# Kernel optimization log

Hardware: AMD Instinct MI355X
Metric: run time of the kernel (lower is better)

## Reference

```python
import jax, jax.numpy as jnp
import numpy as np

D_STATE = 16
D_CONV = 4


def mamba(u, in_w, conv_w, conv_b, x_w, dt_w, dt_b, A_log, Dp, out_w):
    """Standard Mamba block. u: (B, L, d_model)."""
    Bsz, L, _ = u.shape
    xz = u @ in_w.T                      # (B, L, 2*d_inner)
    d_in = xz.shape[-1] // 2
    x, z = xz[..., :d_in], xz[..., d_in:]
    # causal depthwise conv along L
    xt = x.transpose(0, 2, 1)            # (B, d_in, L)
    k = conv_w[:, None, :]               # (d_in, 1, d_conv)
    xt = jax.lax.conv_general_dilated(xt, k, (1,), [(D_CONV - 1, 0)],
                                      feature_group_count=d_in)
    x = jax.nn.silu(xt.transpose(0, 2, 1) + conv_b)
    dbl = x @ x_w.T                      # (B, L, dt_rank + 2*d_state)
    dt_rank = dt_w.shape[1]
    dt = jax.nn.softplus(dbl[..., :dt_rank] @ dt_w.T + dt_b)  # (B, L, d_in)
    Bm = dbl[..., dt_rank:dt_rank + D_STATE]                   # (B, L, n)
    Cm = dbl[..., dt_rank + D_STATE:]                          # (B, L, n)
    A = -jnp.exp(A_log)                                        # (d_in, n)
    dA = jnp.exp(jnp.einsum('bld,dn->bldn', dt, A))            # (B, L, d_in, n)
    dBu = jnp.einsum('bld,bln->bldn', dt * x, Bm)              # (B, L, d_in, n)

    def step(h, inp):
        dA_t, dBu_t, C_t = inp
        h = dA_t * h + dBu_t                                   # (B, d_in, n)
        y = jnp.einsum('bdn,bn->bd', h, C_t)
        return h, y

    h0 = jnp.zeros((Bsz, d_in, D_STATE), u.dtype)
    _, ys = jax.lax.scan(step, h0, (dA.transpose(1, 0, 2, 3),
                                    dBu.transpose(1, 0, 2, 3),
                                    Cm.transpose(1, 0, 2)))
    y = ys.transpose(1, 0, 2) + x * Dp                         # skip connection
    y = y * jax.nn.silu(z)
    return y @ out_w.T


def _mamba_params(key, d_model):
    d_in = 2 * d_model
    dt_rank = max(1, -(-d_model // 16))
    ks = jax.random.split(key, 6)
    s = lambda n: 1.0 / np.sqrt(n)
    p = {
        'in_w': jax.random.normal(ks[0], (2 * d_in, d_model)) * s(d_model),
        'conv_w': jax.random.normal(ks[1], (d_in, D_CONV)) * s(D_CONV),
        'conv_b': jnp.zeros((d_in,)),
        'x_w': jax.random.normal(ks[2], (dt_rank + 2 * D_STATE, d_in)) * s(d_in),
        'dt_w': jax.random.normal(ks[3], (d_in, dt_rank)) * s(dt_rank),
        'dt_b': jax.random.uniform(ks[4], (d_in,), minval=-4.0, maxval=-2.0),
        'A_log': jnp.log(jnp.tile(jnp.arange(1.0, D_STATE + 1.0)[None, :], (d_in, 1))),
        'D': jnp.ones((d_in,)),
        'out_w': jax.random.normal(ks[5], (d_model, d_in)) * s(d_in),
    }
    return p


def setup_inputs() -> dict:
    key = jax.random.key(0)
    kf1, kf2, km1, km2 = jax.random.split(key, 4)
    B, C, H, W = 4, 32, 64, 64
    inp = {
        'fo1': jax.random.normal(kf1, (B, C, H, W), jnp.float32),
        'fo2': jax.random.normal(kf2, (B, C, H, W), jnp.float32),
    }
    for pref, kk, dm in (('m1_', km1, 4 * C), ('m2_', km2, 2)):
        for name, v in _mamba_params(kk, dm).items():
            inp[pref + name] = v.astype(jnp.float32)
    return inp


def reference(fo1, fo2,
              m1_in_w, m1_conv_w, m1_conv_b, m1_x_w, m1_dt_w, m1_dt_b, m1_A_log, m1_D, m1_out_w,
              m2_in_w, m2_conv_w, m2_conv_b, m2_x_w, m2_dt_w, m2_dt_b, m2_A_log, m2_D, m2_out_w):
    B, C, H, W = fo1.shape
    # four directional line-scan sequences, each (B, H*W, C)
    h_fwd = fo1.reshape(B, C, H * W).transpose(0, 2, 1)
    h_bwd = jnp.flip(h_fwd, axis=1)
    w_fwd = fo1.transpose(0, 1, 3, 2).reshape(B, C, H * W).transpose(0, 2, 1)
    w_bwd = jnp.flip(w_fwd, axis=1)
    fop = jnp.concatenate([h_fwd, h_bwd, w_fwd, w_bwd], axis=2)   # (B, HW, 4C)
    fop = mamba(fop, m1_in_w, m1_conv_w, m1_conv_b, m1_x_w, m1_dt_w,
                m1_dt_b, m1_A_log, m1_D, m1_out_w)
    fop = fop.reshape(B, H * W, 4, C).sum(2)                      # (B, HW, C)
    fop = fop.transpose(0, 2, 1).reshape(B, C, H, W)
    residual = fop * fo2
    foc = residual.mean(axis=(2, 3)).reshape(B, C, 1)             # adaptive avg pool (1,1)
    foc = jnp.concatenate([foc, jnp.flip(foc, axis=1)], axis=2)   # (B, C, 2)
    foc = mamba(foc, m2_in_w, m2_conv_w, m2_conv_b, m2_x_w, m2_dt_w,
                m2_dt_b, m2_A_log, m2_D, m2_out_w)
    foc = foc.sum(2, keepdims=True)[..., None]                    # (B, C, 1, 1)
    return foc * residual + residual
```

## Files before the change

kernel.cpp:

```cpp
#include <hip/hip_runtime.h>
#include <cstdint>
#include <cstddef>

constexpr int NCH = 128;
constexpr int TCH = 32;

typedef __attribute__((ext_vector_type(8))) short bf16x8;
typedef __attribute__((ext_vector_type(4))) float f32x4;

static __device__ __forceinline__ float sigm_(float x) { return 1.0f / (1.0f + __expf(-x)); }
static __device__ __forceinline__ float silu_(float x) { return x * sigm_(x); }
static __device__ __forceinline__ float softplus_(float x) { return (x > 20.0f) ? x : log1pf(__expf(x)); }
static __device__ __forceinline__ unsigned short f2bf(float f) {
    union { float f; unsigned int u; } v; v.f = f;
    unsigned int r = v.u + 0x7FFFu + ((v.u >> 16) & 1u);
    return (unsigned short)(r >> 16);
}

__global__ void k_prep(const float* __restrict__ alog1, const float* __restrict__ alog2,
                       const float* __restrict__ w_in, const float* __restrict__ w_x,
                       const float* __restrict__ w_o,
                       float* __restrict__ A2m1, float* __restrict__ A2m2,
                       unsigned short* __restrict__ win_bf, unsigned short* __restrict__ wx_bf,
                       unsigned short* __restrict__ wo_bf, float* __restrict__ foc0) {
    int i = blockIdx.x * 256 + threadIdx.x;
    const float LOG2E = 1.4426950408889634f;
    if (i < 4096)        A2m1[i] = -__expf(alog1[i]) * LOG2E;
    else if (i < 4160)   A2m2[i - 4096] = -__expf(alog2[i - 4096]) * LOG2E;
    else if (i < 69696)  win_bf[i - 4160]  = f2bf(w_in[i - 4160]);
    else if (i < 79936)  wx_bf[i - 69696]  = f2bf(w_x[i - 69696]);
    else if (i < 112704) wo_bf[i - 79936]  = f2bf(w_o[i - 79936]);
    else if (i < 112832) foc0[i - 112704]  = 0.0f;
}

__global__ __launch_bounds__(256) void k_gather(const float* __restrict__ fo1, unsigned short* __restrict__ u) {
    __shared__ float lds[32][65];
    int blk = blockIdx.x;
    int b = blk >> 6, h = blk & 63;
    int tid = threadIdx.x;
    {
        int w = tid & 63, cs = tid >> 6;
        const float* src = fo1 + (size_t)(b * 32) * 4096 + h * 64 + w;
        #pragma unroll
        for (int j = 0; j < 8; ++j) {
            int c = cs * 8 + j;
            lds[c][w] = src[(size_t)c * 4096];
        }
    }
    __syncthreads();
    {
        int c = tid & 31, wsub = tid >> 5;
        #pragma unroll
        for (int j = 0; j < 8; ++j) {
            int w = wsub * 8 + j;
            unsigned short v = f2bf(lds[c][w]);
            int l  = h * 64 + w;
            int l2 = w * 64 + h;
            u[(size_t)(b * 4096 + l)        * 128 +       c] = v;
            u[(size_t)(b * 4096 + 4095 - l) * 128 + 32  + c] = v;
            u[(size_t)(b * 4096 + l2)       * 128 + 64  + c] = v;
            u[(size_t)(b * 4096 + 4095 - l2)* 128 + 96  + c] = v;
        }
    }
}

__global__ __launch_bounds__(256) void k_gemm_mfma(const unsigned short* __restrict__ A,
                                                   const unsigned short* __restrict__ W,
                                                   float* __restrict__ Cmat, int M, int N, int K) {
    __shared__ unsigned short As[128][40];
    __shared__ unsigned short Ws[128][40];
    int n0 = blockIdx.x * 128, m0 = blockIdx.y * 128;
    int tid = threadIdx.x;
    int lane = tid & 63, wv = tid >> 6;
    int mh = wv >> 1, nh = wv & 1;
    int lm = lane & 15, quad = lane >> 4;

    f32x4 acc[4][4];
    #pragma unroll
    for (int i = 0; i < 4; ++i)
        #pragma unroll
        for (int j = 0; j < 4; ++j) acc[i][j] = (f32x4)(0.0f);

    for (int k0 = 0; k0 < K; k0 += 32) {
        #pragma unroll
        for (int j = 0; j < 2; ++j) {
            int c = tid + 256 * j;
            int row = c >> 2;
            int kc = (c & 3) * 8;
            uint4 av = *(const uint4*)&A[(size_t)(m0 + row) * K + k0 + kc];
            *(uint4*)&As[row][kc] = av;
            uint4 wvv = make_uint4(0u, 0u, 0u, 0u);
            if (n0 + row < N) wvv = *(const uint4*)&W[(size_t)(n0 + row) * K + k0 + kc];
            *(uint4*)&Ws[row][kc] = wvv;
        }
        __syncthreads();
        bf16x8 a_frag[4], b_frag[4];
        #pragma unroll
        for (int i = 0; i < 4; ++i)
            a_frag[i] = *(const bf16x8*)&As[mh * 64 + 16 * i + lm][quad * 8];
        #pragma unroll
        for (int j = 0; j < 4; ++j)
            b_frag[j] = *(const bf16x8*)&Ws[nh * 64 + 16 * j + lm][quad * 8];
        #pragma unroll
        for (int i = 0; i < 4; ++i)
            #pragma unroll
            for (int j = 0; j < 4; ++j)
                acc[i][j] = __builtin_amdgcn_mfma_f32_16x16x32_bf16(a_frag[i], b_frag[j], acc[i][j], 0, 0, 0);
        __syncthreads();
    }
    #pragma unroll
    for (int i = 0; i < 4; ++i) {
        #pragma unroll
        for (int r = 0; r < 4; ++r) {
            size_t mrow = (size_t)(m0 + mh * 64 + 16 * i + quad * 4 + r) * N;
            #pragma unroll
            for (int j = 0; j < 4; ++j) {
                int col = n0 + nh * 64 + 16 * j + lm;
                if (col < N) Cmat[mrow + col] = acc[i][j][r];
            }
        }
    }
}

__global__ __launch_bounds__(256) void k_conv(const float* __restrict__ xz, const float* __restrict__ cw,
                                              const float* __restrict__ cb, float* __restrict__ x,
                                              unsigned short* __restrict__ xbf) {
    int blk = blockIdx.x;
    int b = blk >> 7, lc = blk & 127;
    int d = threadIdx.x;
    int l0 = lc * 32;
    float w0 = cw[d * 4 + 0], w1 = cw[d * 4 + 1], w2 = cw[d * 4 + 2], w3 = cw[d * 4 + 3];
    float bb = cb[d];
    size_t rbase = ((size_t)(b * 4096 + l0)) * 512 + d;
    float xm1 = (l0 >= 1) ? xz[rbase - 512]  : 0.f;
    float xm2 = (l0 >= 2) ? xz[rbase - 1024] : 0.f;
    float xm3 = (l0 >= 3) ? xz[rbase - 1536] : 0.f;
    size_t wbase = ((size_t)(b * 4096 + l0)) * 256 + d;
    for (int il = 0; il < 32; ++il) {
        float xc = xz[rbase + (size_t)il * 512];
        float v = silu_(bb + w3 * xc + w2 * xm1 + w1 * xm2 + w0 * xm3);
        x[wbase + (size_t)il * 256] = v;
        xbf[wbase + (size_t)il * 256] = f2bf(v);
        xm3 = xm2; xm2 = xm1; xm1 = xc;
    }
}

__global__ __launch_bounds__(256) void k_scan1(const float* __restrict__ x, const float* __restrict__ dbl,
                                               const float* __restrict__ A2, const float* __restrict__ dtw,
                                               const float* __restrict__ dtb,
                                               float* __restrict__ P, float* __restrict__ S) {
    int blk = blockIdx.x;
    int b = blk / NCH, ch = blk % NCH;
    int d = threadIdx.x;
    float wdt[8];
    #pragma unroll
    for (int r = 0; r < 8; ++r) wdt[r] = dtw[d * 8 + r];
    float bdt = dtb[d];
    float a2[16], h[16], p[16];
    #pragma unroll
    for (int n = 0; n < 16; ++n) { a2[n] = A2[d * 16 + n]; h[n] = 0.f; p[n] = 1.f; }
    int t0 = ch * TCH;
    for (int t = t0; t < t0 + TCH; ++t) {
        size_t row = (size_t)(b * 4096 + t);
        const float* br = dbl + row * 40;
        float4 q0 = *(const float4*)(br), q1 = *(const float4*)(br + 4);
        float4 b0 = *(const float4*)(br + 8), b1 = *(const float4*)(br + 12),
               b2 = *(const float4*)(br + 16), b3 = *(const float4*)(br + 20);
        float dtv = softplus_(q0.x * wdt[0] + q0.y * wdt[1] + q0.z * wdt[2] + q0.w * wdt[3] +
                              q1.x * wdt[4] + q1.y * wdt[5] + q1.z * wdt[6] + q1.w * wdt[7] + bdt);
        float xv = x[row * 256 + d];
        float bm[16] = {b0.x, b0.y, b0.z, b0.w, b1.x, b1.y, b1.z, b1.w,
                        b2.x, b2.y, b2.z, b2.w, b3.x, b3.y, b3.z, b3.w};
        float dx = dtv * xv;
        #pragma unroll
        for (int n = 0; n < 16; ++n) {
            float a = exp2f(dtv * a2[n]);
            h[n] = a * h[n] + dx * bm[n];
            p[n] *= a;
        }
    }
    size_t o = ((size_t)blk * 256 + d) * 16;
    #pragma unroll
    for (int n = 0; n < 16; n += 4) {
        *(float4*)&P[o + n] = make_float4(p[n], p[n + 1], p[n + 2], p[n + 3]);
        *(float4*)&S[o + n] = make_float4(h[n], h[n + 1], h[n + 2], h[n + 3]);
    }
}

__global__ __launch_bounds__(256) void k_scan2(const float* __restrict__ P, const float* S, float* carry) {
    __shared__ float Pl[2048];
    __shared__ float Sl[2048];
    int blk = blockIdx.x;
    int b = blk >> 8, d = blk & 255;
    int tid = threadIdx.x;
    int n = tid & 15, chb = tid >> 4;
    #pragma unroll
    for (int g = 0; g < 8; ++g) {
        int ch = g * 16 + chb;
        size_t o = (((size_t)(b * NCH + ch)) * 256 + d) * 16 + n;
        Pl[ch * 16 + n] = P[o];
        Sl[ch * 16 + n] = S[o];
    }
    __syncthreads();
    for (int st = 1; st < NCH; st <<= 1) {
        float np[8], ns[8];
        #pragma unroll
        for (int g = 0; g < 8; ++g) {
            int ch = g * 16 + chb;
            int i = ch * 16 + n;
            float pc = Pl[i], sc = Sl[i];
            if (ch >= st) {
                float pp = Pl[i - st * 16], sp = Sl[i - st * 16];
                np[g] = pp * pc;
                ns[g] = sp * pc + sc;
            } else { np[g] = pc; ns[g] = sc; }
        }
        __syncthreads();
        #pragma unroll
        for (int g = 0; g < 8; ++g) {
            int i = (g * 16 + chb) * 16 + n;
            Pl[i] = np[g]; Sl[i] = ns[g];
        }
        __syncthreads();
    }
    #pragma unroll
    for (int g = 0; g < 8; ++g) {
        int ch = g * 16 + chb;
        size_t o = (((size_t)(b * NCH + ch)) * 256 + d) * 16 + n;
        carry[o] = (ch == 0) ? 0.f : Sl[(ch - 1) * 16 + n];
    }
}

__global__ __launch_bounds__(256) void k_scan3(const float* __restrict__ x, const float* __restrict__ xz,
                                               const float* __restrict__ dbl, const float* __restrict__ A2,
                                               const float* __restrict__ dtw, const float* __restrict__ dtb,
                                               const float* __restrict__ carry, const float* __restrict__ Dp,
                                               unsigned short* __restrict__ y) {
    int blk = blockIdx.x;
    int b = blk / NCH, ch = blk % NCH;
    int d = threadIdx.x;
    float wdt[8];
    #pragma unroll
    for (int r = 0; r < 8; ++r) wdt[r] = dtw[d * 8 + r];
    float bdt = dtb[d];
    float a2[16], h[16];
    size_t co = ((size_t)blk * 256 + d) * 16;
    #pragma unroll
    for (int n = 0; n < 16; n += 4) {
        float4 v = *(const float4*)&carry[co + n];
        h[n] = v.x; h[n + 1] = v.y; h[n + 2] = v.z; h[n + 3] = v.w;
    }
    #pragma unroll
    for (int n = 0; n < 16; ++n) a2[n] = A2[d * 16 + n];
    float Dd = Dp[d];
    int t0 = ch * TCH;
    for (int t = t0; t < t0 + TCH; ++t) {
        size_t row = (size_t)(b * 4096 + t);
        const float* br = dbl + row * 40;
        float4 q0 = *(const float4*)(br), q1 = *(const float4*)(br + 4);
        float4 b0 = *(const float4*)(br + 8),  b1 = *(const float4*)(br + 12),
               b2 = *(const float4*)(br + 16), b3 = *(const float4*)(br + 20);
        float4 c0 = *(const float4*)(br + 24), c1 = *(const float4*)(br + 28),
               c2 = *(const float4*)(br + 32), c3 = *(const float4*)(br + 36);
        float dtv = softplus_(q0.x * wdt[0] + q0.y * wdt[1] + q0.z * wdt[2] + q0.w * wdt[3] +
                              q1.x * wdt[4] + q1.y * wdt[5] + q1.z * wdt[6] + q1.w * wdt[7] + bdt);
        float xv = x[row * 256 + d];
        float zv = xz[row * 512 + 256 + d];
        float bm[16] = {b0.x, b0.y, b0.z, b0.w, b1.x, b1.y, b1.z, b1.w,
                        b2.x, b2.y, b2.z, b2.w, b3.x, b3.y, b3.z, b3.w};
        float cm[16] = {c0.x, c0.y, c0.z, c0.w, c1.x, c1.y, c1.z, c1.w,
                        c2.x, c2.y, c2.z, c2.w, c3.x, c3.y, c3.z, c3.w};
        float dx = dtv * xv;
        float yv = 0.f;
        #pragma unroll
        for (int n = 0; n < 16; ++n) {
            float a = exp2f(dtv * a2[n]);
            h[n] = a * h[n] + dx * bm[n];
            yv += h[n] * cm[n];
        }
        yv = (yv + xv * Dd) * silu_(zv);
        y[row * 256 + d] = f2bf(yv);
    }
}

__global__ __launch_bounds__(256) void k_oproj(const unsigned short* __restrict__ A,
                                               const unsigned short* __restrict__ W,
                                               const float* __restrict__ fo2,
                                               float* __restrict__ res, float* __restrict__ foc0) {
    __shared__ unsigned short As[128][40];
    __shared__ unsigned short Ws[128][40];
    __shared__ float gs[2][128][37];
    int m0 = blockIdx.x * 128;
    int b = m0 >> 12, l0 = m0 & 4095;
    int tid = threadIdx.x;
    int lane = tid & 63, wv = tid >> 6;
    int mh = wv >> 1, nh = wv & 1;
    int lm = lane & 15, quad = lane >> 4;

    f32x4 acc[4][4];
    #pragma unroll
    for (int i = 0; i < 4; ++i)
        #pragma unroll
        for (int j = 0; j < 4; ++j) acc[i][j] = (f32x4)(0.0f);

    for (int k0 = 0; k0 < 256; k0 += 32) {
        #pragma unroll
        for (int j = 0; j < 2; ++j) {
            int c = tid + 256 * j;
            int row = c >> 2;
            int kc = (c & 3) * 8;
            *(uint4*)&As[row][kc] = *(const uint4*)&A[(size_t)(m0 + row) * 256 + k0 + kc];
            *(uint4*)&Ws[row][kc] = *(const uint4*)&W[(size_t)row * 256 + k0 + kc];
        }
        __syncthreads();
        bf16x8 a_frag[4], b_frag[4];
        #pragma unroll
        for (int i = 0; i < 4; ++i)
            a_frag[i] = *(const bf16x8*)&As[mh * 64 + 16 * i + lm][quad * 8];
        #pragma unroll
        for (int j = 0; j < 4; ++j)
            b_frag[j] = *(const bf16x8*)&Ws[nh * 64 + 16 * j + lm][quad * 8];
        #pragma unroll
        for (int i = 0; i < 4; ++i)
            #pragma unroll
            for (int j = 0; j < 4; ++j)
                acc[i][j] = __builtin_amdgcn_mfma_f32_16x16x32_bf16(a_frag[i], b_frag[j], acc[i][j], 0, 0, 0);
        __syncthreads();
    }
    #pragma unroll
    for (int i = 0; i < 4; ++i) {
        #pragma unroll
        for (int r = 0; r < 4; ++r) {
            int lr = mh * 64 + 16 * i + quad * 4 + r;
            gs[nh][lr][lm]      = acc[i][0][r] + acc[i][2][r];
            gs[nh][lr][lm + 16] = acc[i][1][r] + acc[i][3][r];
        }
    }
    __syncthreads();
    {
        int c = tid >> 3, i8 = tid & 7;
        float psum = 0.f;
        size_t obase = ((size_t)(b * 32 + c)) * 4096 + l0;
        #pragma unroll
        for (int ii = 0; ii < 16; ++ii) {
            int lr = i8 * 16 + ii;
            float v = (gs[0][lr][c] + gs[1][lr][c]) * fo2[obase + lr];
            res[obase + lr] = v;
            psum += v;
        }
        psum += __shfl_xor(psum, 1, 64);
        psum += __shfl_xor(psum, 2, 64);
        psum += __shfl_xor(psum, 4, 64);
        if (i8 == 0) atomicAdd(&foc0[b * 32 + c], psum);
    }
}

__global__ __launch_bounds__(256) void k_mamba2(const float* __restrict__ foc0,
                                                const float* __restrict__ in_w, const float* __restrict__ cw,
                                                const float* __restrict__ cb, const float* __restrict__ xw,
                                                const float* __restrict__ dtw, const float* __restrict__ dtb,
                                                const float* __restrict__ A2, const float* __restrict__ Dp,
                                                const float* __restrict__ ow, float* __restrict__ focf) {
    __shared__ float xz2[4][32][8];
    __shared__ float x2c[4][32][4];
    __shared__ float dbl2[4][32][33];
    __shared__ float dt2[4][32][4];
    __shared__ float y2[4][32][4];
    int tid = threadIdx.x;
    const float SC = 1.0f / 4096.0f;
    for (int i = tid; i < 4 * 32 * 8; i += 256) {
        int b = i >> 8, l = (i >> 3) & 31, j = i & 7;
        float u0 = foc0[b * 32 + l] * SC, u1 = foc0[b * 32 + 31 - l] * SC;
        xz2[b][l][j] = u0 * in_w[j * 2] + u1 * in_w[j * 2 + 1];
    }
    __syncthreads();
    for (int i = tid; i < 4 * 32 * 4; i += 256) {
        int b = i >> 7, l = (i >> 2) & 31, d = i & 3;
        float acc = cb[d] + cw[d * 4 + 3] * xz2[b][l][d];
        if (l >= 1) acc += cw[d * 4 + 2] * xz2[b][l - 1][d];
        if (l >= 2) acc += cw[d * 4 + 1] * xz2[b][l - 2][d];
        if (l >= 3) acc += cw[d * 4 + 0] * xz2[b][l - 3][d];
        x2c[b][l][d] = silu_(acc);
    }
    __syncthreads();
    for (int i = tid; i < 4 * 32 * 33; i += 256) {
        int b = i / (32 * 33); int rem = i % (32 * 33); int l = rem / 33; int j = rem % 33;
        float s = 0.f;
        #pragma unroll
        for (int d = 0; d < 4; ++d) s += x2c[b][l][d] * xw[j * 4 + d];
        dbl2[b][l][j] = s;
    }
    __syncthreads();
    for (int i = tid; i < 4 * 32 * 4; i += 256) {
        int b = i >> 7, l = (i >> 2) & 31, d = i & 3;
        dt2[b][l][d] = softplus_(dbl2[b][l][0] * dtw[d] + dtb[d]);
    }
    __syncthreads();
    {
        int b = tid >> 6, d = (tid >> 4) & 3, n = tid & 15;
        float a2v = A2[d * 16 + n];
        float h = 0.f;
        for (int t = 0; t < 32; ++t) {
            float dtv = dt2[b][t][d];
            float a = exp2f(dtv * a2v);
            h = a * h + dtv * x2c[b][t][d] * dbl2[b][t][1 + n];
            float contrib = h * dbl2[b][t][17 + n];
            contrib += __shfl_xor(contrib, 1, 64);
            contrib += __shfl_xor(contrib, 2, 64);
            contrib += __shfl_xor(contrib, 4, 64);
            contrib += __shfl_xor(contrib, 8, 64);
            if (n == 0) y2[b][t][d] = contrib;
        }
    }
    __syncthreads();
    if (tid < 128) {
        int b = tid >> 5, l = tid & 31;
        float s = 0.f;
        #pragma unroll
        for (int d = 0; d < 4; ++d) {
            float yg = (y2[b][l][d] + x2c[b][l][d] * Dp[d]) * silu_(xz2[b][l][4 + d]);
            s += yg * (ow[d] + ow[4 + d]);
        }
        focf[b * 32 + l] = s;
    }
}

__global__ __launch_bounds__(256) void k_final(const float* __restrict__ res, const float* __restrict__ focf,
                                               float* __restrict__ out) {
    int i = blockIdx.x * 256 + threadIdx.x;
    int bc = i >> 12;
    out[i] = res[i] * (1.0f + focf[bc]);
}

extern "C" void kernel_launch(void* const* d_in, const int* in_sizes, int n_in,
                              void* d_out, int out_size, void* d_ws, size_t ws_size,
                              hipStream_t stream) {
    const float* fo1      = (const float*)d_in[0];
    const float* fo2      = (const float*)d_in[1];
    const float* m1_in_w  = (const float*)d_in[2];
    const float* m1_cw    = (const float*)d_in[3];
    const float* m1_cb    = (const float*)d_in[4];
    const float* m1_xw    = (const float*)d_in[5];
    const float* m1_dtw   = (const float*)d_in[6];
    const float* m1_dtb   = (const float*)d_in[7];
    const float* m1_alog  = (const float*)d_in[8];
    const float* m1_D     = (const float*)d_in[9];
    const float* m1_ow    = (const float*)d_in[10];
    const float* m2_in_w  = (const float*)d_in[11];
    const float* m2_cw    = (const float*)d_in[12];
    const float* m2_cb    = (const float*)d_in[13];
    const float* m2_xw    = (const float*)d_in[14];
    const float* m2_dtw   = (const float*)d_in[15];
    const float* m2_dtb   = (const float*)d_in[16];
    const float* m2_alog  = (const float*)d_in[17];
    const float* m2_D     = (const float*)d_in[18];
    const float* m2_ow    = (const float*)d_in[19];

    float* ws = (float*)d_ws;
    unsigned short* u_bf = (unsigned short*)ws;
    float* xz    = ws + 1048576;
    float* xbuf  = ws + 9437184;
    unsigned short* xbf = (unsigned short*)(ws + 13631488);
    float* dbl   = ws + 15728640;
    float* Pb    = ws + 16384000;
    float* Sb    = ws + 18481152;
    unsigned short* ybf = (unsigned short*)Pb;
    float* carry = Sb;
    float* res   = ws + 20578304;
    float* foc0  = ws + 21102592;
    float* focf  = ws + 21102720;
    float* A2m1  = ws + 21102848;
    float* A2m2  = ws + 21106944;
    unsigned short* win_bf = (unsigned short*)(ws + 21107008);
    unsigned short* wx_bf  = (unsigned short*)(ws + 21139776);
    unsigned short* wo_bf  = (unsigned short*)(ws + 21144896);

    k_prep<<<441, 256, 0, stream>>>(m1_alog, m2_alog, m1_in_w, m1_xw, m1_ow,
                                    A2m1, A2m2, win_bf, wx_bf, wo_bf, foc0);
    k_gather<<<256, 256, 0, stream>>>(fo1, u_bf);
    {   dim3 g(4, 128);  k_gemm_mfma<<<g, 256, 0, stream>>>(u_bf, win_bf, xz, 16384, 512, 128); }
    k_conv<<<512, 256, 0, stream>>>(xz, m1_cw, m1_cb, xbuf, xbf);
    {   dim3 g(1, 128);  k_gemm_mfma<<<g, 256, 0, stream>>>(xbf, wx_bf, dbl, 16384, 40, 256); }
    k_scan1<<<4 * NCH, 256, 0, stream>>>(xbuf, dbl, A2m1, m1_dtw, m1_dtb, Pb, Sb);
    k_scan2<<<1024, 256, 0, stream>>>(Pb, Sb, carry);
    k_scan3<<<4 * NCH, 256, 0, stream>>>(xbuf, xz, dbl, A2m1, m1_dtw, m1_dtb, carry, m1_D, ybf);
    k_oproj<<<128, 256, 0, stream>>>(ybf, wo_bf, fo2, res, foc0);
    k_mamba2<<<1, 256, 0, stream>>>(foc0, m2_in_w, m2_cw, m2_cb, m2_xw, m2_dtw, m2_dtb,
                                    A2m2, m2_D, m2_ow, focf);
    k_final<<<2048, 256, 0, stream>>>(res, focf, (float*)d_out);
}
```

Before: 261.7 us.

## Precompute dt, drop fp32 x buffer, double scan chunks, derive chunk decay from dt sum

```diff
diff --git a/kernel.cpp b/kernel.cpp
--- a/kernel.cpp
+++ b/kernel.cpp
@@ -2,8 +2,8 @@
 #include <cstdint>
 #include <cstddef>
 
-constexpr int NCH = 128;
-constexpr int TCH = 32;
+constexpr int NCH = 256;
+constexpr int TCH = 16;
 
 typedef __attribute__((ext_vector_type(8))) short bf16x8;
 typedef __attribute__((ext_vector_type(4))) float f32x4;
@@ -15,6 +15,10 @@
     union { float f; unsigned int u; } v; v.f = f;
     unsigned int r = v.u + 0x7FFFu + ((v.u >> 16) & 1u);
     return (unsigned short)(r >> 16);
+}
+static __device__ __forceinline__ float bf2f(unsigned short s) {
+    union { unsigned int u; float f; } v; v.u = ((unsigned int)s) << 16;
+    return v.f;
 }
 
 __global__ void k_prep(const float* __restrict__ alog1, const float* __restrict__ alog2,
@@ -123,7 +127,7 @@
 }
 
 __global__ __launch_bounds__(256) void k_conv(const float* __restrict__ xz, const float* __restrict__ cw,
-                                              const float* __restrict__ cb, float* __restrict__ x,
+                                              const float* __restrict__ cb,
                                               unsigned short* __restrict__ xbf) {
     int blk = blockIdx.x;
     int b = blk >> 7, lc = blk & 127;
@@ -139,63 +143,71 @@
     for (int il = 0; il < 32; ++il) {
         float xc = xz[rbase + (size_t)il * 512];
         float v = silu_(bb + w3 * xc + w2 * xm1 + w1 * xm2 + w0 * xm3);
-        x[wbase + (size_t)il * 256] = v;
         xbf[wbase + (size_t)il * 256] = f2bf(v);
         xm3 = xm2; xm2 = xm1; xm1 = xc;
     }
 }
 
-__global__ __launch_bounds__(256) void k_scan1(const float* __restrict__ x, const float* __restrict__ dbl,
-                                               const float* __restrict__ A2, const float* __restrict__ dtw,
-                                               const float* __restrict__ dtb,
+__global__ __launch_bounds__(256) void k_dtproj(const float* __restrict__ dbl, const float* __restrict__ dtw,
+                                                const float* __restrict__ dtb, float* __restrict__ dt) {
+    int blk = blockIdx.x;
+    int d = threadIdx.x;
+    const float* r = dbl + (size_t)blk * 40;
+    float4 q0 = *(const float4*)(r);
+    float4 q1 = *(const float4*)(r + 4);
+    float4 w0 = *(const float4*)(dtw + d * 8);
+    float4 w1 = *(const float4*)(dtw + d * 8 + 4);
+    float v = q0.x * w0.x + q0.y * w0.y + q0.z * w0.z + q0.w * w0.w +
+              q1.x * w1.x + q1.y * w1.y + q1.z * w1.z + q1.w * w1.w + dtb[d];
+    dt[(size_t)blk * 256 + d] = softplus_(v);
+}
+
+__global__ __launch_bounds__(256) void k_scan1(const float* __restrict__ dt, const unsigned short* __restrict__ xbf,
+                                               const float* __restrict__ dbl, const float* __restrict__ A2,
                                                float* __restrict__ P, float* __restrict__ S) {
     int blk = blockIdx.x;
-    int b = blk / NCH, ch = blk % NCH;
+    int b = blk >> 8, ch = blk & 255;
     int d = threadIdx.x;
-    float wdt[8];
-    #pragma unroll
-    for (int r = 0; r < 8; ++r) wdt[r] = dtw[d * 8 + r];
-    float bdt = dtb[d];
-    float a2[16], h[16], p[16];
-    #pragma unroll
-    for (int n = 0; n < 16; ++n) { a2[n] = A2[d * 16 + n]; h[n] = 0.f; p[n] = 1.f; }
+    float a2[16], h[16];
+    #pragma unroll
+    for (int n = 0; n < 16; ++n) { a2[n] = A2[d * 16 + n]; h[n] = 0.f; }
+    float sdt = 0.f;
     int t0 = ch * TCH;
     for (int t = t0; t < t0 + TCH; ++t) {
         size_t row = (size_t)(b * 4096 + t);
-        const float* br = dbl + row * 40;
-        float4 q0 = *(const float4*)(br), q1 = *(const float4*)(br + 4);
-        float4 b0 = *(const float4*)(br + 8), b1 = *(const float4*)(br + 12),
-               b2 = *(const float4*)(br + 16), b3 = *(const float4*)(br + 20);
-        float dtv = softplus_(q0.x * wdt[0] + q0.y * wdt[1] + q0.z * wdt[2] + q0.w * wdt[3] +
-                              q1.x * wdt[4] + q1.y * wdt[5] + q1.z * wdt[6] + q1.w * wdt[7] + bdt);
-        float xv = x[row * 256 + d];
+        float dtv = dt[row * 256 + d];
+        float xv  = bf2f(xbf[row * 256 + d]);
+        const float* br = dbl + row * 40 + 8;
+        float4 b0 = *(const float4*)(br), b1 = *(const float4*)(br + 4),
+               b2 = *(const float4*)(br + 8), b3 = *(const float4*)(br + 12);
         float bm[16] = {b0.x, b0.y, b0.z, b0.w, b1.x, b1.y, b1.z, b1.w,
                         b2.x, b2.y, b2.z, b2.w, b3.x, b3.y, b3.z, b3.w};
         float dx = dtv * xv;
+        sdt += dtv;
         #pragma unroll
         for (int n = 0; n < 16; ++n) {
             float a = exp2f(dtv * a2[n]);
             h[n] = a * h[n] + dx * bm[n];
-            p[n] *= a;
         }
     }
     size_t o = ((size_t)blk * 256 + d) * 16;
     #pragma unroll
     for (int n = 0; n < 16; n += 4) {
-        *(float4*)&P[o + n] = make_float4(p[n], p[n + 1], p[n + 2], p[n + 3]);
+        *(float4*)&P[o + n] = make_float4(exp2f(a2[n] * sdt), exp2f(a2[n + 1] * sdt),
+                                          exp2f(a2[n + 2] * sdt), exp2f(a2[n + 3] * sdt));
         *(float4*)&S[o + n] = make_float4(h[n], h[n + 1], h[n + 2], h[n + 3]);
     }
 }
 
 __global__ __launch_bounds__(256) void k_scan2(const float* __restrict__ P, const float* S, float* carry) {
-    __shared__ float Pl[2048];
-    __shared__ float Sl[2048];
+    __shared__ float Pl[NCH * 16];
+    __shared__ float Sl[NCH * 16];
     int blk = blockIdx.x;
     int b = blk >> 8, d = blk & 255;
     int tid = threadIdx.x;
     int n = tid & 15, chb = tid >> 4;
     #pragma unroll
-    for (int g = 0; g < 8; ++g) {
+    for (int g = 0; g < 16; ++g) {
         int ch = g * 16 + chb;
         size_t o = (((size_t)(b * NCH + ch)) * 256 + d) * 16 + n;
         Pl[ch * 16 + n] = P[o];
@@ -203,9 +215,9 @@
     }
     __syncthreads();
     for (int st = 1; st < NCH; st <<= 1) {
-        float np[8], ns[8];
-        #pragma unroll
-        for (int g = 0; g < 8; ++g) {
+        float np[16], ns[16];
+        #pragma unroll
+        for (int g = 0; g < 16; ++g) {
             int ch = g * 16 + chb;
             int i = ch * 16 + n;
             float pc = Pl[i], sc = Sl[i];
@@ -217,32 +229,27 @@
         }
         __syncthreads();
         #pragma unroll
-        for (int g = 0; g < 8; ++g) {
+        for (int g = 0; g < 16; ++g) {
             int i = (g * 16 + chb) * 16 + n;
             Pl[i] = np[g]; Sl[i] = ns[g];
         }
         __syncthreads();
     }
     #pragma unroll
-    for (int g = 0; g < 8; ++g) {
+    for (int g = 0; g < 16; ++g) {
         int ch = g * 16 + chb;
         size_t o = (((size_t)(b * NCH + ch)) * 256 + d) * 16 + n;
         carry[o] = (ch == 0) ? 0.f : Sl[(ch - 1) * 16 + n];
     }
 }
 
-__global__ __launch_bounds__(256) void k_scan3(const float* __restrict__ x, const float* __restrict__ xz,
-                                               const float* __restrict__ dbl, const float* __restrict__ A2,
-                                               const float* __restrict__ dtw, const float* __restrict__ dtb,
-                                               const float* __restrict__ carry, const float* __restrict__ Dp,
-                                               unsigned short* __restrict__ y) {
-    int blk = blockIdx.x;
-    int b = blk / NCH, ch = blk % NCH;
+__global__ __launch_bounds__(256) void k_scan3(const float* __restrict__ dt, const unsigned short* __restrict__ xbf,
+                                               const float* __restrict__ xz, const float* __restrict__ dbl,
+                                               const float* __restrict__ A2, const float* __restrict__ carry,
+                                               const float* __restrict__ Dp, unsigned short* __restrict__ y) {
+    int blk = blockIdx.x;
+    int b = blk >> 8, ch = blk & 255;
     int d = threadIdx.x;
-    float wdt[8];
-    #pragma unroll
-    for (int r = 0; r < 8; ++r) wdt[r] = dtw[d * 8 + r];
-    float bdt = dtb[d];
     float a2[16], h[16];
     size_t co = ((size_t)blk * 256 + d) * 16;
     #pragma unroll
@@ -256,16 +263,14 @@
     int t0 = ch * TCH;
     for (int t = t0; t < t0 + TCH; ++t) {
         size_t row = (size_t)(b * 4096 + t);
-        const float* br = dbl + row * 40;
-        float4 q0 = *(const float4*)(br), q1 = *(const float4*)(br + 4);
-        float4 b0 = *(const float4*)(br + 8),  b1 = *(const float4*)(br + 12),
-               b2 = *(const float4*)(br + 16), b3 = *(const float4*)(br + 20);
-        float4 c0 = *(const float4*)(br + 24), c1 = *(const float4*)(br + 28),
-               c2 = *(const float4*)(br + 32), c3 = *(const float4*)(br + 36);
-        float dtv = softplus_(q0.x * wdt[0] + q0.y * wdt[1] + q0.z * wdt[2] + q0.w * wdt[3] +
-                              q1.x * wdt[4] + q1.y * wdt[5] + q1.z * wdt[6] + q1.w * wdt[7] + bdt);
-        float xv = x[row * 256 + d];
-        float zv = xz[row * 512 + 256 + d];
+        float dtv = dt[row * 256 + d];
+        float xv  = bf2f(xbf[row * 256 + d]);
+        float zv  = xz[row * 512 + 256 + d];
+        const float* br = dbl + row * 40 + 8;
+        float4 b0 = *(const float4*)(br),      b1 = *(const float4*)(br + 4),
+               b2 = *(const float4*)(br + 8),  b3 = *(const float4*)(br + 12);
+        float4 c0 = *(const float4*)(br + 16), c1 = *(const float4*)(br + 20),
+               c2 = *(const float4*)(br + 24), c3 = *(const float4*)(br + 28);
         float bm[16] = {b0.x, b0.y, b0.z, b0.w, b1.x, b1.y, b1.z, b1.w,
                         b2.x, b2.y, b2.z, b2.w, b3.x, b3.y, b3.z, b3.w};
         float cm[16] = {c0.x, c0.y, c0.z, c0.w, c1.x, c1.y, c1.z, c1.w,
@@ -459,31 +464,34 @@
     float* ws = (float*)d_ws;
     unsigned short* u_bf = (unsigned short*)ws;
     float* xz    = ws + 1048576;
-    float* xbuf  = ws + 9437184;
-    unsigned short* xbf = (unsigned short*)(ws + 13631488);
-    float* dbl   = ws + 15728640;
+    unsigned short* xbf = (unsigned short*)(ws + 9437184);
+    float* dbl   = ws + 11534336;
+    float* dtbuf = ws + 12189696;
     float* Pb    = ws + 16384000;
-    float* Sb    = ws + 18481152;
+    float* Sb    = ws + 20578304;
     unsigned short* ybf = (unsigned short*)Pb;
     float* carry = Sb;
-    float* res   = ws + 20578304;
-    float* foc0  = ws + 21102592;
-    float* focf  = ws + 21102720;
-    float* A2m1  = ws + 21102848;
-    float* A2m2  = ws + 21106944;
-    unsigned short* win_bf = (unsigned short*)(ws + 21107008);
-    unsigned short* wx_bf  = (unsigned short*)(ws + 21139776);
-    unsigned short* wo_bf  = (unsigned short*)(ws + 21144896);
+    float* opre  = xz;
+    (void)opre;
+    float* res   = ws + 24772608;
+    float* foc0  = ws + 25296896;
+    float* focf  = ws + 25297024;
+    float* A2m1  = ws + 25297152;
+    float* A2m2  = ws + 25301248;
+    unsigned short* win_bf = (unsigned short*)(ws + 25301312);
+    unsigned short* wx_bf  = (unsigned short*)(ws + 25334080);
+    unsigned short* wo_bf  = (unsigned short*)(ws + 25339200);
 
     k_prep<<<441, 256, 0, stream>>>(m1_alog, m2_alog, m1_in_w, m1_xw, m1_ow,
                                     A2m1, A2m2, win_bf, wx_bf, wo_bf, foc0);
     k_gather<<<256, 256, 0, stream>>>(fo1, u_bf);
     {   dim3 g(4, 128);  k_gemm_mfma<<<g, 256, 0, stream>>>(u_bf, win_bf, xz, 16384, 512, 128); }
-    k_conv<<<512, 256, 0, stream>>>(xz, m1_cw, m1_cb, xbuf, xbf);
+    k_conv<<<512, 256, 0, stream>>>(xz, m1_cw, m1_cb, xbf);
     {   dim3 g(1, 128);  k_gemm_mfma<<<g, 256, 0, stream>>>(xbf, wx_bf, dbl, 16384, 40, 256); }
-    k_scan1<<<4 * NCH, 256, 0, stream>>>(xbuf, dbl, A2m1, m1_dtw, m1_dtb, Pb, Sb);
+    k_dtproj<<<16384, 256, 0, stream>>>(dbl, m1_dtw, m1_dtb, dtbuf);
+    k_scan1<<<4 * NCH, 256, 0, stream>>>(dtbuf, xbf, dbl, A2m1, Pb, Sb);
     k_scan2<<<1024, 256, 0, stream>>>(Pb, Sb, carry);
-    k_scan3<<<4 * NCH, 256, 0, stream>>>(xbuf, xz, dbl, A2m1, m1_dtw, m1_dtb, carry, m1_D, ybf);
+    k_scan3<<<4 * NCH, 256, 0, stream>>>(dtbuf, xbf, xz, dbl, A2m1, carry, m1_D, ybf);
     k_oproj<<<128, 256, 0, stream>>>(ybf, wo_bf, fo2, res, foc0);
     k_mamba2<<<1, 256, 0, stream>>>(foc0, m2_in_w, m2_cw, m2_cb, m2_xw, m2_dtw, m2_dtb,
                                     A2m2, m2_D, m2_ow, focf);
```

Result: faster. 249.2 us (-4.8%).
